# Optimization experiments

Hardware: AMD Instinct MI355X
Metric: run time of the kernel (lower is better)

Reference implementation:

```python
import jax, jax.numpy as jnp
import numpy as np

N, L, C_IN, NOISE_C, COMP, NC = 64, 1024, 514, 64, 16, 3
MAIN_C = COMP + NOISE_C  # 80

def _conv1d(x, w, b):
    # x: [N, Cin, L], w: [Cout, Cin, K] -> 'same' padding conv, stride 1
    k = w.shape[-1]
    y = jax.lax.conv_general_dilated(x, w, (1,), [(k // 2, k // 2)],
                                     dimension_numbers=('NCH', 'OIH', 'NCH'))
    return y + b[None, :, None]

def _bn(x, gamma, beta, eps=1e-5):
    # training-mode BatchNorm1d: biased batch stats over (N, L)
    mu = jnp.mean(x, axis=(0, 2), keepdims=True)
    var = jnp.var(x, axis=(0, 2), keepdims=True)
    return (x - mu) * jax.lax.rsqrt(var + eps) * gamma[None, :, None] + beta[None, :, None]

def _lrelu(x):
    return jax.nn.leaky_relu(x, 0.2)

def _pos_encode(length, dim, dtype):
    d = jnp.arange(dim)
    div = 1.0 / jnp.power(10000.0, (2.0 * (d // 2).astype(dtype)) / dim)  # [dim]
    ang = div[:, None] * jnp.arange(length, dtype=dtype)[None, :]          # [dim, L]
    pe = jnp.where((d % 2 == 0)[:, None], jnp.sin(ang), jnp.cos(ang))
    return pe[None].astype(dtype)  # [1, dim, L]

def _label_revise(probs):
    # Vectorized equivalent of the per-sample Python revision loop
    # (circle_itv=2, slider_itv=4, stride=2). Output length == input length.
    # Row j semantics (m = 4*(j//4), chain(m) = pred[m]==2 and pred[m+4]==2 and m+4<L):
    #   j%4==0: always probs[j]
    #   chain(m) and j%4!=0: pad [0,0,1]
    #   j%4==1 (not chain): pred[m] in {1,2} -> [1,0,0] else probs[j]
    #   j%4==2 (not chain): probs[j]
    #   j%4==3 (not chain): pred[j-1]==1 -> [1,0,0] else probs[j]
    n, l, c = probs.shape
    pred = jnp.argmax(probs, axis=-1)                 # [N, L]
    pred_b = pred[:, ::4]                              # pred at multiples of 4
    nxt = jnp.concatenate([pred_b[:, 1:], jnp.full((n, 1), -1, pred_b.dtype)], axis=1)
    chain = jnp.repeat((pred_b == 2) & (nxt == 2), 4, axis=1)   # [N, L]
    predm = jnp.repeat(pred_b, 4, axis=1)                        # [N, L]
    phase = jnp.arange(l) % 4
    prev = jnp.concatenate([jnp.zeros((n, 1), pred.dtype), pred[:, :-1]], axis=1)
    pad100 = jnp.array([1.0, 0.0, 0.0], probs.dtype)
    pad001 = jnp.array([0.0, 0.0, 1.0], probs.dtype)
    c100 = (((phase == 1)[None] & ((predm == 1) | (predm == 2)))
            | ((phase == 3)[None] & (prev == 1))) & ~chain
    out = jnp.where(c100[..., None], pad100, probs)
    out = jnp.where((chain & (phase != 0)[None])[..., None], pad001, out)
    return out

def _forward(noise, cond_data, gumbel, ew1, eb1, ew2, eb2, eg, ebt,
             w3, b3, w4, b4, g4, bt4, lw1, lb1, lw2, lb2, lw3, lb3):
    # FeatureExtractor
    x = jnp.swapaxes(cond_data, 1, 2)                       # [N, 514, L]
    x = _lrelu(_conv1d(x, ew1, eb1))                        # [N, 32, L]
    cond = _bn(_conv1d(x, ew2, eb2), eg, ebt)               # [N, 16, L] (no act)
    # main generator
    gi = jnp.concatenate([cond, jnp.swapaxes(noise, 1, 2)], axis=1)  # [N, 80, L]
    gi = gi + _pos_encode(L, MAIN_C, gi.dtype)
    h = _lrelu(_conv1d(gi, w3, b3))                         # [N, 48, L]
    h = _lrelu(_bn(_conv1d(h, w4, b4), g4, bt4))            # [N, 12, L]
    h = h.reshape(h.shape[0], -1)                           # [N, 12*L]
    h = _lrelu(h @ lw1 + lb1)
    h = _lrelu(h @ lw2 + lb2)
    logits = (h @ lw3 + lb3).reshape(-1, L, NC)             # [N, L, 3]
    rev = _label_revise(logits)
    # hard gumbel-softmax (tau=1) with straight-through estimator
    y_soft = jax.nn.softmax(rev + gumbel, axis=-1)
    y_hard = jax.nn.one_hot(jnp.argmax(y_soft, axis=-1), NC, dtype=y_soft.dtype)
    gen = y_hard + y_soft - jax.lax.stop_gradient(y_soft)
    return gen, cond

def setup_inputs() -> dict:
    key = jax.random.key(0)
    ks = jax.random.split(key, 12)
    s = jnp.float32(0.02)
    return {
        'noise': jax.random.normal(ks[0], (N, L, NOISE_C), jnp.float32),
        'cond_data': jax.random.normal(ks[1], (N, L, C_IN), jnp.float32),
        'gumbel': jax.random.gumbel(ks[2], (N, L, NC), jnp.float32),
        'ew1': jax.random.normal(ks[3], (C_IN // 16, C_IN, 1), jnp.float32) * s,
        'eb1': jnp.zeros((C_IN // 16,), jnp.float32),
        'ew2': jax.random.normal(ks[4], (COMP, C_IN // 16, 3), jnp.float32) * s,
        'eb2': jnp.zeros((COMP,), jnp.float32),
        'eg': jnp.ones((COMP,), jnp.float32),
        'ebt': jnp.zeros((COMP,), jnp.float32),
        'w3': jax.random.normal(ks[5], (NC * 16, MAIN_C, 7), jnp.float32) * s,
        'b3': jnp.zeros((NC * 16,), jnp.float32),
        'w4': jax.random.normal(ks[6], (NC * 4, NC * 16, 3), jnp.float32) * s,
        'b4': jnp.zeros((NC * 4,), jnp.float32),
        'g4': jnp.ones((NC * 4,), jnp.float32),
        'bt4': jnp.zeros((NC * 4,), jnp.float32),
        'lw1': jax.random.normal(ks[7], (NC * 4 * L, NC * L), jnp.float32) * s,
        'lb1': jnp.zeros((NC * L,), jnp.float32),
        'lw2': jax.random.normal(ks[8], (NC * L, NC * L), jnp.float32) * s,
        'lb2': jnp.zeros((NC * L,), jnp.float32),
        'lw3': jax.random.normal(ks[9], (NC * L, NC * L), jnp.float32) * s,
        'lb3': jnp.zeros((NC * L,), jnp.float32),
    }

def reference(noise, cond_data, gumbel, ew1, eb1, ew2, eb2, eg, ebt,
              w3, b3, w4, b4, g4, bt4, lw1, lb1, lw2, lb2, lw3, lb3):
    return _forward(noise, cond_data, gumbel, ew1, eb1, ew2, eb2, eg, ebt,
                    w3, b3, w4, b4, g4, bt4, lw1, lb1, lw2, lb2, lw3, lb3)
```

## Files before the change

kernel.cpp:

```cpp
#include <hip/hip_runtime.h>
#include <hip/hip_bf16.h>
#include <math.h>


__device__ __forceinline__ float lrelu(float x){ return fmaxf(x, 0.2f*x); }

__global__ void k_init(const float* __restrict__ ew1, const float* __restrict__ ew2,
                       const float* __restrict__ w3,  const float* __restrict__ w4,
                       float* __restrict__ wT1, float* __restrict__ wT2,
                       float* __restrict__ wT3, float* __restrict__ wT4,
                       float* __restrict__ pe){
  int i = blockIdx.x*256 + threadIdx.x;
  if (i < 16448){
    int c = i>>5, oc = i&31;
    wT1[i] = ew1[oc*514 + c];
  } else if (i < 16448+1536){
    int j = i - 16448; int oc = j%16; int t = j/16; int dl = t%3; int ic = t/3;
    wT2[j] = ew2[(oc*32+ic)*3 + dl];
  } else if (i < 16448+1536+26880){
    int j = i - 17984; int oc = j%48; int t = j/48; int dl = t%7; int ic = t/7;
    wT3[j] = w3[(oc*80+ic)*7 + dl];
  } else if (i < 46592){
    int j = i - 44864; int oc = j%12; int t = j/12; int dl = t%3; int ic = t/3;
    wT4[j] = w4[(oc*48+ic)*3 + dl];
  } else if (i < 46592 + 80*1024){
    int j = i - 46592;
    int ch = j >> 10, l = j & 1023;
    double dv = 1.0 / pow(10000.0, (2.0*(double)(ch>>1)) / 80.0);
    double ang = dv * (double)l;
    pe[j] = (float)((ch & 1) ? cos(ang) : sin(ang));
  }
}

__global__ __launch_bounds__(256) void k_conv1(const float* __restrict__ A,
    const float* __restrict__ wT1, const float* __restrict__ eb1,
    float* __restrict__ x1){
  __shared__ float red[32][256];
  const int tid = threadIdx.x;
  const int pl  = tid & 63;
  const int s   = __builtin_amdgcn_readfirstlane(tid >> 6);
  const int p   = blockIdx.x*64 + pl;

  const int c0 = (s == 0) ? 0 : 130 + (s-1)*128;
  const int c1 = (s == 0) ? 130 : 130 + s*128;

  const float* row = A + (size_t)p*514;
  float acc[32];
  #pragma unroll
  for (int j=0;j<32;j++) acc[j]=0.f;

  #pragma unroll 8
  for (int c=c0;c<c1;c+=2){
    float2 v = *reinterpret_cast<const float2*>(row + c);
    const float* w = wT1 + (size_t)c*32;
    #pragma unroll
    for (int j=0;j<32;j++) acc[j] = fmaf(v.x, w[j],    acc[j]);
    #pragma unroll
    for (int j=0;j<32;j++) acc[j] = fmaf(v.y, w[32+j], acc[j]);
  }

  #pragma unroll
  for (int j=0;j<32;j++) red[j][s*64 + pl] = acc[j];
  __syncthreads();

  float out[8];
  #pragma unroll
  for (int j=0;j<8;j++){
    const int c = s*8 + j;
    float v = (red[c][pl] + red[c][64+pl]) + (red[c][128+pl] + red[c][192+pl]);
    out[j] = lrelu(v + eb1[c]);
  }
  float* dst = x1 + ((size_t)(blockIdx.x*64 + pl))*32 + s*8;
  *(float4*)(dst  ) = make_float4(out[0],out[1],out[2],out[3]);
  *(float4*)(dst+4) = make_float4(out[4],out[5],out[6],out[7]);
}

__global__ __launch_bounds__(256) void k_conv2(const float* __restrict__ x1,
    const float* __restrict__ wT2, const float* __restrict__ eb2,
    float* __restrict__ y2, float* __restrict__ part){
  __shared__ float xt[32][264];
  const int tid = threadIdx.x, lane = tid & 63;
  const int wv = __builtin_amdgcn_readfirstlane(tid >> 6);
  const int n = blockIdx.x >> 2, base = (blockIdx.x & 3)*256;

  for (int r = tid; r < 264; r += 256){
    int l = base - 4 + r;
    if (l >= 0 && l < 1024){
      const float* src = x1 + ((size_t)n*1024 + l)*32;
      #pragma unroll
      for (int c=0;c<32;c+=4){
        float4 v = *(const float4*)(src + c);
        xt[c][r]=v.x; xt[c+1][r]=v.y; xt[c+2][r]=v.z; xt[c+3][r]=v.w;
      }
    } else {
      #pragma unroll
      for (int c=0;c<32;c++) xt[c][r] = 0.f;
    }
  }
  __syncthreads();

  const int og = wv*4;
  const int j0 = 4*lane;
  float acc[4][4];
  #pragma unroll
  for (int j=0;j<4;j++){
    #pragma unroll
    for (int p=0;p<4;p++) acc[j][p]=0.f;
  }
  for (int ic=0; ic<32; ic++){
    float xr[12];
    #pragma unroll
    for (int u=0;u<12;u+=4){
      float4 v = *(const float4*)&xt[ic][j0+u];
      xr[u]=v.x; xr[u+1]=v.y; xr[u+2]=v.z; xr[u+3]=v.w;
    }
    const float* wrow = wT2 + ic*48 + og;
    #pragma unroll
    for (int dl=0;dl<3;dl++){
      #pragma unroll
      for (int j=0;j<4;j++){
        float w = wrow[dl*16 + j];
        #pragma unroll
        for (int p=0;p<4;p++)
          acc[j][p] = fmaf(xr[p+dl+3], w, acc[j][p]);
      }
    }
  }
  float s[4], q[4];
  #pragma unroll
  for (int j=0;j<4;j++){ s[j]=0.f; q[j]=0.f; }
  const int l0 = base + 4*lane;
  #pragma unroll
  for (int p=0;p<4;p++){
    float vv[4];
    #pragma unroll
    for (int j=0;j<4;j++){
      float val = acc[j][p] + eb2[og+j];
      vv[j]=val; s[j]+=val; q[j]+=val*val;
    }
    *(float4*)(y2 + ((size_t)n*1024 + l0 + p)*16 + og) = make_float4(vv[0],vv[1],vv[2],vv[3]);
  }
  #pragma unroll
  for (int off=32; off; off>>=1){
    #pragma unroll
    for (int j=0;j<4;j++){ s[j] += __shfl_xor(s[j], off); q[j] += __shfl_xor(q[j], off); }
  }
  if (lane == 0){
    #pragma unroll
    for (int j=0;j<4;j++){
      part[((size_t)blockIdx.x*16 + og + j)*2    ] = s[j];
      part[((size_t)blockIdx.x*16 + og + j)*2 + 1] = q[j];
    }
  }
}

__global__ __launch_bounds__(256) void k_conv3(const float* __restrict__ y2,
    const float* __restrict__ noise, const float* __restrict__ pe,
    const float* __restrict__ bn2p, const float* __restrict__ eg,
    const float* __restrict__ ebt,
    const float* __restrict__ wT3, const float* __restrict__ b3,
    float* __restrict__ h3, float* __restrict__ cond_out){
  __shared__ float xt[80][72];
  __shared__ double pS[16][16], pQ[16][16];
  __shared__ float ssh[32];
  const int tid = threadIdx.x, lane = tid & 63;
  const int og = __builtin_amdgcn_readfirstlane(tid >> 6) * 12;
  const int n = blockIdx.x >> 4, base = (blockIdx.x & 15)*64;

  {
    int c = tid & 15, chunk = tid >> 4;
    double S=0.0, Q=0.0;
    #pragma unroll 4
    for (int i=chunk*16; i<chunk*16+16; i++){
      S += (double)bn2p[((size_t)i*16 + c)*2];
      Q += (double)bn2p[((size_t)i*16 + c)*2 + 1];
    }
    pS[chunk][c] = S; pQ[chunk][c] = Q;
  }
  __syncthreads();
  if (tid < 16){
    double S=0.0, Q=0.0;
    #pragma unroll
    for (int k=0;k<16;k++){ S += pS[k][tid]; Q += pQ[k][tid]; }
    double mean = S / 65536.0;
    double var  = Q / 65536.0 - mean*mean;
    double sc   = (double)eg[tid] / sqrt(var + 1e-5);
    ssh[tid*2]   = (float)sc;
    ssh[tid*2+1] = (float)((double)ebt[tid] - mean*sc);
  }
  __syncthreads();

  {
    const int q = tid & 3;
    for (int r = tid >> 2; r < 72; r += 64){
      int l = base - 4 + r;
      bool valid = (l >= 0 && l < 1024);
      if (q == 0){
        if (valid){
          size_t p = (size_t)n*1024 + l;
          const float* ys = y2 + p*16;
          bool interior = (r >= 4 && r < 68);
          #pragma unroll
          for (int c=0;c<16;c++){
            float cv = fmaf(ys[c], ssh[2*c], ssh[2*c+1]);
            if (interior) cond_out[((size_t)n*16 + c)*1024 + l] = cv;
            xt[c][r] = cv + pe[c*1024 + l];
          }
          const float* ns = noise + p*64;
          #pragma unroll
          for (int c=0;c<4;c++)
            xt[16+c][r] = ns[c] + pe[(16+c)*1024 + l];
        } else {
          #pragma unroll
          for (int c=0;c<20;c++) xt[c][r] = 0.f;
        }
      } else {
        if (valid){
          size_t p = (size_t)n*1024 + l;
          const float* ns = noise + p*64 + (q*20 - 16);
          #pragma unroll
          for (int c=0;c<20;c++)
            xt[q*20 + c][r] = ns[c] + pe[(q*20 + c)*1024 + l];
        } else {
          #pragma unroll
          for (int c=0;c<20;c++) xt[q*20 + c][r] = 0.f;
        }
      }
    }
  }
  __syncthreads();

  float acc[12];
  #pragma unroll
  for (int j=0;j<12;j++) acc[j]=0.f;
  for (int ic=0; ic<80; ic++){
    float xr[7];
    #pragma unroll
    for (int u=0;u<7;u++) xr[u] = xt[ic][lane+1+u];
    const float* wrow = wT3 + ic*336 + og;
    #pragma unroll
    for (int dl=0;dl<7;dl++){
      #pragma unroll
      for (int j=0;j<12;j++)
        acc[j] = fmaf(xr[dl], wrow[dl*48 + j], acc[j]);
    }
  }
  {
    float v[12];
    #pragma unroll
    for (int j=0;j<12;j++) v[j] = lrelu(acc[j] + b3[og+j]);
    float* dst = h3 + ((size_t)n*1024 + base + lane)*48 + og;
    *(float4*)(dst  ) = make_float4(v[0],v[1],v[2],v[3]);
    *(float4*)(dst+4) = make_float4(v[4],v[5],v[6],v[7]);
    *(float4*)(dst+8) = make_float4(v[8],v[9],v[10],v[11]);
  }
}

__global__ __launch_bounds__(256) void k_conv4(const float* __restrict__ h3,
    const float* __restrict__ wT4, const float* __restrict__ b4,
    float* __restrict__ y4, float* __restrict__ part){
  __shared__ float xt[48][258];
  __shared__ float red[4][24];
  const int tid = threadIdx.x, lane = tid & 63, wv = tid >> 6;
  const int n = blockIdx.x >> 2, base = (blockIdx.x & 3)*256;

  for (int r = tid; r < 258; r += 256){
    int l = base - 1 + r;
    if (l >= 0 && l < 1024){
      const float* src = h3 + ((size_t)n*1024 + l)*48;
      #pragma unroll
      for (int c=0;c<48;c+=4){
        float4 v = *(const float4*)(src + c);
        xt[c][r]=v.x; xt[c+1][r]=v.y; xt[c+2][r]=v.z; xt[c+3][r]=v.w;
      }
    } else {
      #pragma unroll
      for (int c=0;c<48;c++) xt[c][r]=0.f;
    }
  }
  __syncthreads();

  float acc[12];
  #pragma unroll
  for (int j=0;j<12;j++) acc[j]=0.f;
  for (int ic=0; ic<48; ic++){
    float x0 = xt[ic][tid], x1v = xt[ic][tid+1], x2 = xt[ic][tid+2];
    const float* wrow = wT4 + ic*36;
    #pragma unroll
    for (int j=0;j<12;j++){
      acc[j] = fmaf(x0,  wrow[j],      acc[j]);
      acc[j] = fmaf(x1v, wrow[12 + j], acc[j]);
      acc[j] = fmaf(x2,  wrow[24 + j], acc[j]);
    }
  }
  float s[12], q[12];
  #pragma unroll
  for (int j=0;j<12;j++){
    float v = acc[j] + b4[j];
    acc[j] = v; s[j] = v; q[j] = v*v;
  }
  {
    float* dst = y4 + ((size_t)n*1024 + base + tid)*12;
    *(float4*)(dst  ) = make_float4(acc[0],acc[1],acc[2],acc[3]);
    *(float4*)(dst+4) = make_float4(acc[4],acc[5],acc[6],acc[7]);
    *(float4*)(dst+8) = make_float4(acc[8],acc[9],acc[10],acc[11]);
  }
  #pragma unroll
  for (int off=32; off; off>>=1){
    #pragma unroll
    for (int j=0;j<12;j++){ s[j] += __shfl_xor(s[j], off); q[j] += __shfl_xor(q[j], off); }
  }
  if (lane == 0){
    #pragma unroll
    for (int j=0;j<12;j++){ red[wv][j] = s[j]; red[wv][12+j] = q[j]; }
  }
  __syncthreads();
  if (tid < 24){
    float v = red[0][tid] + red[1][tid] + red[2][tid] + red[3][tid];
    if (tid < 12) part[((size_t)blockIdx.x*12 + tid)*2] = v;
    else          part[((size_t)blockIdx.x*12 + (tid-12))*2 + 1] = v;
  }
}

__global__ __launch_bounds__(256) void k_hflat(const float* __restrict__ y4,
    const float* __restrict__ bn4p, const float* __restrict__ g4,
    const float* __restrict__ bt4, float* __restrict__ hT){
  __shared__ double pS[16][12], pQ[16][12];
  __shared__ float ssh[24];
  const int tid = threadIdx.x;
  if (tid < 192){
    int c = tid % 12, chunk = tid / 12;
    double S=0.0, Q=0.0;
    #pragma unroll 4
    for (int i=chunk*16; i<chunk*16+16; i++){
      S += (double)bn4p[((size_t)i*12 + c)*2];
      Q += (double)bn4p[((size_t)i*12 + c)*2 + 1];
    }
    pS[chunk][c] = S; pQ[chunk][c] = Q;
  }
  __syncthreads();
  if (tid < 12){
    double S=0.0, Q=0.0;
    #pragma unroll
    for (int k=0;k<16;k++){ S += pS[k][tid]; Q += pQ[k][tid]; }
    double mean = S / 65536.0;
    double var  = Q / 65536.0 - mean*mean;
    double sc   = (double)g4[tid] / sqrt(var + 1e-5);
    ssh[tid*2]   = (float)sc;
    ssh[tid*2+1] = (float)((double)bt4[tid] - mean*sc);
  }
  __syncthreads();

  int nn = tid & 63;
  int l  = blockIdx.x*4 + (tid >> 6);
  const float* src = y4 + ((size_t)nn*1024 + l)*12;
  #pragma unroll
  for (int c=0;c<12;c++){
    float v = lrelu(fmaf(src[c], ssh[2*c], ssh[2*c+1]));
    hT[((size_t)(c*1024 + l))*64 + nn] = v;
  }
}

__global__ __launch_bounds__(256) void k_fc2(const float* __restrict__ AT,
    const float* __restrict__ W, float* __restrict__ part,
    int nsplit, int kwave){
  __shared__ float red[64][64];
  const int lane = threadIdx.x & 63;
  const int w  = __builtin_amdgcn_readfirstlane(threadIdx.x >> 6);
  const int sk = w >> 1;
  const int mh = (w & 1) * 32;
  const int s  = blockIdx.x % nsplit;
  const int ot = blockIdx.x / nsplit;
  const int o  = ot*64 + lane;
  const int k0 = (s*2 + sk) * kwave;

  float acc[32];
  #pragma unroll
  for (int m=0;m<32;m++) acc[m]=0.f;

  const float* ap = AT + (size_t)k0*64 + mh;
  const float* wp = W  + (size_t)k0*3072 + o;

  float wb[8];
  #pragma unroll
  for (int u=0;u<8;u++) wb[u] = wp[(size_t)u*3072];

  for (int k=0; k<kwave-8; k+=8){
    float wn[8];
    const float* wpn = wp + (size_t)(k+8)*3072;
    #pragma unroll
    for (int u=0;u<8;u++) wn[u] = wpn[(size_t)u*3072];
    #pragma unroll
    for (int u=0;u<8;u++){
      const float* a = ap + (size_t)(k+u)*64;
      #pragma unroll
      for (int m=0;m<32;m++) acc[m] = fmaf(a[m], wb[u], acc[m]);
    }
    #pragma unroll
    for (int u=0;u<8;u++) wb[u] = wn[u];
  }
  #pragma unroll
  for (int u=0;u<8;u++){
    const float* a = ap + (size_t)(kwave-8+u)*64;
    #pragma unroll
    for (int m=0;m<32;m++) acc[m] = fmaf(a[m], wb[u], acc[m]);
  }

  if (sk == 1){
    #pragma unroll
    for (int m=0;m<32;m++) red[mh + m][lane] = acc[m];
  }
  __syncthreads();
  if (sk == 0){
    float* dst = part + (size_t)s*64*3072 + o;
    #pragma unroll
    for (int m=0;m<32;m++){
      acc[m] += red[mh + m][lane];
      dst[(size_t)(mh + m)*3072] = acc[m];
    }
  }
}

__global__ __launch_bounds__(256) void k_fcreduce(const float* __restrict__ part,
    const float* __restrict__ bias, float* __restrict__ out,
    int S, int act, int transposed){
  const int ot = blockIdx.x >> 4;
  const int mg = blockIdx.x & 15;
  const int lane = threadIdx.x & 63;
  const int o = ot*64 + lane;
  const int m = mg*4 + (threadIdx.x >> 6);
  float v = 0.f;
  for (int s=0;s<S;s++) v += part[((size_t)s*64 + m)*3072 + o];
  v += bias[o];
  if (act) v = fmaxf(v, 0.2f*v);
  if (transposed) out[(size_t)o*64 + m] = v;
  else            out[(size_t)m*3072 + o] = v;
}

__global__ __launch_bounds__(256) void k_label(const float* __restrict__ logits,
    const float* __restrict__ gumbel, float* __restrict__ out){
  __shared__ int pred[1024];
  const int n = blockIdx.x;
  const float* lg = logits + (size_t)n*3072;
  for (int l = threadIdx.x; l < 1024; l += 256){
    float a = lg[l*3], b = lg[l*3+1], c = lg[l*3+2];
    int pm = 0; float bv = a;
    if (b > bv){ pm = 1; bv = b; }
    if (c > bv){ pm = 2; }
    pred[l] = pm;
  }
  __syncthreads();
  const float* gm = gumbel + (size_t)n*3072;
  float* op = out + (size_t)n*3072;
  for (int l = threadIdx.x; l < 1024; l += 256){
    int phase = l & 3, lb = l >> 2;
    int pb  = pred[lb*4];
    int nxt = (lb < 255) ? pred[(lb+1)*4] : -1;
    bool chain = (pb == 2) && (nxt == 2);
    int prev = (l > 0) ? pred[l-1] : 0;
    bool c100 = (((phase == 1) && (pb == 1 || pb == 2)) ||
                 ((phase == 3) && (prev == 1))) && !chain;
    float r0, r1, r2;
    if (chain && phase != 0){ r0=0.f; r1=0.f; r2=1.f; }
    else if (c100)          { r0=1.f; r1=0.f; r2=0.f; }
    else { r0 = lg[l*3]; r1 = lg[l*3+1]; r2 = lg[l*3+2]; }
    float z0 = r0 + gm[l*3], z1 = r1 + gm[l*3+1], z2 = r2 + gm[l*3+2];
    int am = 0; float bv = z0;
    if (z1 > bv){ am = 1; bv = z1; }
    if (z2 > bv){ am = 2; }
    op[l*3+0] = (am == 0) ? 1.f : 0.f;
    op[l*3+1] = (am == 1) ? 1.f : 0.f;
    op[l*3+2] = (am == 2) ? 1.f : 0.f;
  }
}

extern "C" void kernel_launch(void* const* d_in, const int* in_sizes, int n_in,
                              void* d_out, int out_size, void* d_ws, size_t ws_size,
                              hipStream_t stream){
  (void)in_sizes; (void)n_in; (void)out_size;
  const float* noise     = (const float*)d_in[0];
  const float* cond_data = (const float*)d_in[1];
  const float* gumbel    = (const float*)d_in[2];
  const float* ew1 = (const float*)d_in[3];
  const float* eb1 = (const float*)d_in[4];
  const float* ew2 = (const float*)d_in[5];
  const float* eb2 = (const float*)d_in[6];
  const float* eg  = (const float*)d_in[7];
  const float* ebt = (const float*)d_in[8];
  const float* w3  = (const float*)d_in[9];
  const float* b3  = (const float*)d_in[10];
  const float* w4  = (const float*)d_in[11];
  const float* b4  = (const float*)d_in[12];
  const float* g4  = (const float*)d_in[13];
  const float* bt4 = (const float*)d_in[14];
  const float* lw1 = (const float*)d_in[15];
  const float* lb1 = (const float*)d_in[16];
  const float* lw2 = (const float*)d_in[17];
  const float* lb2 = (const float*)d_in[18];
  const float* lw3 = (const float*)d_in[19];
  const float* lb3 = (const float*)d_in[20];

  float* ws = (float*)d_ws;
  float* wT1   = ws + 0;
  float* wT2   = ws + 16448;
  float* wT3   = ws + 17984;
  float* wT4   = ws + 44864;
  float* pe    = ws + 46592;
  float* bn2p  = ws + 128512;
  float* bn4p  = ws + 136736;
  float* x1    = ws + 143360;
  float* y2    = ws + 2240512;
  float* h3    = ws + 3289088;
  float* y4    = ws + 6434816;
  float* hT    = ws + 7221248;
  float* fcp   = ws + 8007680;

  int S1 = 32;
  if (ws_size < (size_t)(8007680 + 32*196608 + 3*196608) * 4) S1 = 16;
  const int S23 = 16;
  float* fc1T  = fcp + (size_t)S1*196608;
  float* fc2T  = fc1T + 196608;
  float* logi  = fc2T + 196608;
  const int kw1  = 12288 / (S1*2);
  const int kw23 = 3072 / (S23*2);

  float* out_gen  = (float*)d_out;
  float* out_cond = (float*)d_out + 196608;

  k_init <<<502, 256, 0, stream>>>(ew1, ew2, w3, w4, wT1, wT2, wT3, wT4, pe);
  k_conv1<<<1024, 256, 0, stream>>>(cond_data, wT1, eb1, x1);
  k_conv2<<<256, 256, 0, stream>>>(x1, wT2, eb2, y2, bn2p);
  k_conv3<<<1024, 256, 0, stream>>>(y2, noise, pe, bn2p, eg, ebt, wT3, b3, h3, out_cond);
  k_conv4<<<256, 256, 0, stream>>>(h3, wT4, b4, y4, bn4p);
  k_hflat<<<256, 256, 0, stream>>>(y4, bn4p, g4, bt4, hT);
  k_fc2  <<<48*S1, 256, 0, stream>>>(hT,   lw1, fcp, S1, kw1);
  k_fcreduce<<<768, 256, 0, stream>>>(fcp, lb1, fc1T, S1, 1, 1);
  k_fc2  <<<48*S23, 256, 0, stream>>>(fc1T, lw2, fcp, S23, kw23);
  k_fcreduce<<<768, 256, 0, stream>>>(fcp, lb2, fc2T, S23, 1, 1);
  k_fc2  <<<48*S23, 256, 0, stream>>>(fc2T, lw3, fcp, S23, kw23);
  k_fcreduce<<<768, 256, 0, stream>>>(fcp, lb3, logi, S23, 0, 0);
  k_label<<<64, 256, 0, stream>>>(logi, gumbel, out_gen);
}
```

Measured before the change: 325.2 us.

## Stage FC activation tiles in LDS and deepen FC1 split-K

Adds a new FC kernel that copies the activation slice for its K range into shared memory once per block, then streams weight rows with register double-buffering over a fixed K chunk of 96. FC1 now uses 64 K-splits instead of 32, and FC2/FC3 use the new kernel. The aim is to raise parallelism and cut repeated global reads of activations for these memory-bound GEMVs. In exchange it adds LDS pressure and more partial sums for the reduce kernel to read. It keeps the old kernel as a fallback when the workspace is too small.

```diff
diff --git a/kernel.cpp b/kernel.cpp
--- a/kernel.cpp
+++ b/kernel.cpp
@@ -421,6 +421,78 @@
   }
 }
 
+__global__ __launch_bounds__(256) void k_fc6(const float* __restrict__ AT,
+    const float* __restrict__ W, float* __restrict__ part,
+    int nsplit){
+  const int kwave = 96;
+  __shared__ float als[2*96*64];
+  const int tid  = threadIdx.x;
+  const int lane = tid & 63;
+  const int w  = __builtin_amdgcn_readfirstlane(tid >> 6);
+  const int sk = w >> 1;
+  const int mh = (w & 1) * 32;
+  const int s  = blockIdx.x % nsplit;
+  const int ot = blockIdx.x / nsplit;
+  const int o  = ot*64 + lane;
+  const int k0 = (s*2 + sk) * kwave;
+
+  {
+    const float4* src = (const float4*)(AT + (size_t)(s*2*kwave)*64);
+    float4* dst = (float4*)als;
+    #pragma unroll
+    for (int i=0;i<12;i++)
+      dst[tid + i*256] = src[tid + i*256];
+  }
+  __syncthreads();
+
+  float acc[32];
+  #pragma unroll
+  for (int m=0;m<32;m++) acc[m]=0.f;
+
+  const float* ap = als + (sk*kwave)*64 + mh;
+  const float* wp = W + (size_t)k0*3072 + o;
+
+  float wb[8];
+  #pragma unroll
+  for (int u=0;u<8;u++) wb[u] = wp[(size_t)u*3072];
+
+  for (int k=0; k<kwave-8; k+=8){
+    float wn[8];
+    const float* wpn = wp + (size_t)(k+8)*3072;
+    #pragma unroll
+    for (int u=0;u<8;u++) wn[u] = wpn[(size_t)u*3072];
+    #pragma unroll
+    for (int u=0;u<8;u++){
+      const float* a = ap + (k+u)*64;
+      #pragma unroll
+      for (int m=0;m<32;m++) acc[m] = fmaf(a[m], wb[u], acc[m]);
+    }
+    #pragma unroll
+    for (int u=0;u<8;u++) wb[u] = wn[u];
+  }
+  #pragma unroll
+  for (int u=0;u<8;u++){
+    const float* a = ap + (kwave-8+u)*64;
+    #pragma unroll
+    for (int m=0;m<32;m++) acc[m] = fmaf(a[m], wb[u], acc[m]);
+  }
+
+  __syncthreads();
+  if (sk == 1){
+    #pragma unroll
+    for (int m=0;m<32;m++) als[(mh+m)*64 + lane] = acc[m];
+  }
+  __syncthreads();
+  if (sk == 0){
+    float* dst = part + (size_t)s*64*3072 + o;
+    #pragma unroll
+    for (int m=0;m<32;m++){
+      acc[m] += als[(mh+m)*64 + lane];
+      dst[(size_t)(mh+m)*3072] = acc[m];
+    }
+  }
+}
+
 __global__ __launch_bounds__(256) void k_fcreduce(const float* __restrict__ part,
     const float* __restrict__ bias, float* __restrict__ out,
     int S, int act, int transposed){
@@ -515,14 +587,15 @@
   float* hT    = ws + 7221248;
   float* fcp   = ws + 8007680;
 
-  int S1 = 32;
-  if (ws_size < (size_t)(8007680 + 32*196608 + 3*196608) * 4) S1 = 16;
+  int S1 = 64;
+  bool lds_fc1 = true;
+  if (ws_size < (size_t)(8007680 + (size_t)64*196608 + 3*196608) * 4){
+    S1 = 32; lds_fc1 = false;
+  }
   const int S23 = 16;
   float* fc1T  = fcp + (size_t)S1*196608;
   float* fc2T  = fc1T + 196608;
   float* logi  = fc2T + 196608;
-  const int kw1  = 12288 / (S1*2);
-  const int kw23 = 3072 / (S23*2);
 
   float* out_gen  = (float*)d_out;
   float* out_cond = (float*)d_out + 196608;
@@ -533,11 +606,12 @@
   k_conv3<<<1024, 256, 0, stream>>>(y2, noise, pe, bn2p, eg, ebt, wT3, b3, h3, out_cond);
   k_conv4<<<256, 256, 0, stream>>>(h3, wT4, b4, y4, bn4p);
   k_hflat<<<256, 256, 0, stream>>>(y4, bn4p, g4, bt4, hT);
-  k_fc2  <<<48*S1, 256, 0, stream>>>(hT,   lw1, fcp, S1, kw1);
+  if (lds_fc1) k_fc6<<<48*64, 256, 0, stream>>>(hT, lw1, fcp, 64);
+  else         k_fc2<<<48*32, 256, 0, stream>>>(hT, lw1, fcp, 32, 192);
   k_fcreduce<<<768, 256, 0, stream>>>(fcp, lb1, fc1T, S1, 1, 1);
-  k_fc2  <<<48*S23, 256, 0, stream>>>(fc1T, lw2, fcp, S23, kw23);
+  k_fc6  <<<48*16, 256, 0, stream>>>(fc1T, lw2, fcp, 16);
   k_fcreduce<<<768, 256, 0, stream>>>(fcp, lb2, fc2T, S23, 1, 1);
-  k_fc2  <<<48*S23, 256, 0, stream>>>(fc2T, lw3, fcp, S23, kw23);
+  k_fc6  <<<48*16, 256, 0, stream>>>(fc2T, lw3, fcp, 16);
   k_fcreduce<<<768, 256, 0, stream>>>(fcp, lb3, logi, S23, 0, 0);
   k_label<<<64, 256, 0, stream>>>(logi, gumbel, out_gen);
 }
```

Measured after the change: 380.2 us. +16.9%, slower.

## Stage FC activation tiles in LDS and raise split-K for FC2/FC3

Applied to the files above, without the earlier changes.

The FC GEMV-like kernel now copies 48-row chunks of the transposed activation matrix into shared memory with float4 loads, in phases. Each wave then reads the chunk from LDS rather than re-reading global/L1 per lane. Split-K for the second and third FC layers goes from 16 to 32 to put more blocks on the device. The workspace size fallback is removed, so the code now assumes the workspace is large enough for 32 partials. More syncs and more partial-reduce traffic are added in exchange.

```diff
diff --git a/kernel.cpp b/kernel.cpp
--- a/kernel.cpp
+++ b/kernel.cpp
@@ -361,12 +361,14 @@
   }
 }
 
-__global__ __launch_bounds__(256) void k_fc2(const float* __restrict__ AT,
-    const float* __restrict__ W, float* __restrict__ part,
-    int nsplit, int kwave){
-  __shared__ float red[64][64];
-  const int lane = threadIdx.x & 63;
-  const int w  = __builtin_amdgcn_readfirstlane(threadIdx.x >> 6);
+template<int NPH>
+__global__ __launch_bounds__(256) void k_fc7(const float* __restrict__ AT,
+    const float* __restrict__ W, float* __restrict__ part, int nsplit){
+  const int kwave = NPH*48;
+  __shared__ float als[2*48*64];
+  const int tid  = threadIdx.x;
+  const int lane = tid & 63;
+  const int w  = __builtin_amdgcn_readfirstlane(tid >> 6);
   const int sk = w >> 1;
   const int mh = (w & 1) * 32;
   const int s  = blockIdx.x % nsplit;
@@ -378,45 +380,61 @@
   #pragma unroll
   for (int m=0;m<32;m++) acc[m]=0.f;
 
-  const float* ap = AT + (size_t)k0*64 + mh;
-  const float* wp = W  + (size_t)k0*3072 + o;
-
+  const float* wp = W + (size_t)k0*3072 + o;
   float wb[8];
   #pragma unroll
   for (int u=0;u<8;u++) wb[u] = wp[(size_t)u*3072];
 
-  for (int k=0; k<kwave-8; k+=8){
-    float wn[8];
-    const float* wpn = wp + (size_t)(k+8)*3072;
-    #pragma unroll
-    for (int u=0;u<8;u++) wn[u] = wpn[(size_t)u*3072];
-    #pragma unroll
-    for (int u=0;u<8;u++){
-      const float* a = ap + (size_t)(k+u)*64;
-      #pragma unroll
-      for (int m=0;m<32;m++) acc[m] = fmaf(a[m], wb[u], acc[m]);
-    }
-    #pragma unroll
-    for (int u=0;u<8;u++) wb[u] = wn[u];
-  }
-  #pragma unroll
-  for (int u=0;u<8;u++){
-    const float* a = ap + (size_t)(kwave-8+u)*64;
-    #pragma unroll
-    for (int m=0;m<32;m++) acc[m] = fmaf(a[m], wb[u], acc[m]);
-  }
-
+  for (int ph=0; ph<NPH; ++ph){
+    __syncthreads();
+    {
+      const float4* s0 = (const float4*)(AT + ((size_t)(s*2    )*kwave + ph*48)*64);
+      const float4* s1 = (const float4*)(AT + ((size_t)(s*2 + 1)*kwave + ph*48)*64);
+      float4* d = (float4*)als;
+      #pragma unroll
+      for (int i=0;i<3;i++){
+        d[tid + i*256]       = s0[tid + i*256];
+        d[768 + tid + i*256] = s1[tid + i*256];
+      }
+    }
+    __syncthreads();
+
+    const float* ap = als + sk*48*64 + mh;
+    #pragma unroll
+    for (int g=0; g<6; ++g){
+      const int kk = ph*48 + g*8;
+      float wn[8];
+      const bool pref = (kk + 8 < kwave);
+      if (pref){
+        const float* wpn = wp + (size_t)(kk+8)*3072;
+        #pragma unroll
+        for (int u=0;u<8;u++) wn[u] = wpn[(size_t)u*3072];
+      }
+      #pragma unroll
+      for (int u=0;u<8;u++){
+        const float* a = ap + (g*8+u)*64;
+        #pragma unroll
+        for (int m=0;m<32;m++) acc[m] = fmaf(a[m], wb[u], acc[m]);
+      }
+      if (pref){
+        #pragma unroll
+        for (int u=0;u<8;u++) wb[u] = wn[u];
+      }
+    }
+  }
+
+  __syncthreads();
   if (sk == 1){
     #pragma unroll
-    for (int m=0;m<32;m++) red[mh + m][lane] = acc[m];
+    for (int m=0;m<32;m++) als[(mh+m)*64 + lane] = acc[m];
   }
   __syncthreads();
   if (sk == 0){
     float* dst = part + (size_t)s*64*3072 + o;
     #pragma unroll
     for (int m=0;m<32;m++){
-      acc[m] += red[mh + m][lane];
-      dst[(size_t)(mh + m)*3072] = acc[m];
+      acc[m] += als[(mh+m)*64 + lane];
+      dst[(size_t)(mh+m)*3072] = acc[m];
     }
   }
 }
@@ -477,7 +495,7 @@
 extern "C" void kernel_launch(void* const* d_in, const int* in_sizes, int n_in,
                               void* d_out, int out_size, void* d_ws, size_t ws_size,
                               hipStream_t stream){
-  (void)in_sizes; (void)n_in; (void)out_size;
+  (void)in_sizes; (void)n_in; (void)out_size; (void)ws_size;
   const float* noise     = (const float*)d_in[0];
   const float* cond_data = (const float*)d_in[1];
   const float* gumbel    = (const float*)d_in[2];
@@ -515,14 +533,11 @@
   float* hT    = ws + 7221248;
   float* fcp   = ws + 8007680;
 
-  int S1 = 32;
-  if (ws_size < (size_t)(8007680 + 32*196608 + 3*196608) * 4) S1 = 16;
-  const int S23 = 16;
-  float* fc1T  = fcp + (size_t)S1*196608;
+  const int S1  = 32;
+  const int S23 = 32;
+  float* fc1T  = fcp + (size_t)32*196608;
   float* fc2T  = fc1T + 196608;
   float* logi  = fc2T + 196608;
-  const int kw1  = 12288 / (S1*2);
-  const int kw23 = 3072 / (S23*2);
 
   float* out_gen  = (float*)d_out;
   float* out_cond = (float*)d_out + 196608;
@@ -533,11 +548,11 @@
   k_conv3<<<1024, 256, 0, stream>>>(y2, noise, pe, bn2p, eg, ebt, wT3, b3, h3, out_cond);
   k_conv4<<<256, 256, 0, stream>>>(h3, wT4, b4, y4, bn4p);
   k_hflat<<<256, 256, 0, stream>>>(y4, bn4p, g4, bt4, hT);
-  k_fc2  <<<48*S1, 256, 0, stream>>>(hT,   lw1, fcp, S1, kw1);
+  k_fc7<4><<<48*S1, 256, 0, stream>>>(hT,   lw1, fcp, S1);
   k_fcreduce<<<768, 256, 0, stream>>>(fcp, lb1, fc1T, S1, 1, 1);
-  k_fc2  <<<48*S23, 256, 0, stream>>>(fc1T, lw2, fcp, S23, kw23);
+  k_fc7<1><<<48*S23, 256, 0, stream>>>(fc1T, lw2, fcp, S23);
   k_fcreduce<<<768, 256, 0, stream>>>(fcp, lb2, fc2T, S23, 1, 1);
-  k_fc2  <<<48*S23, 256, 0, stream>>>(fc2T, lw3, fcp, S23, kw23);
+  k_fc7<1><<<48*S23, 256, 0, stream>>>(fc2T, lw3, fcp, S23);
   k_fcreduce<<<768, 256, 0, stream>>>(fcp, lb3, logi, S23, 0, 0);
   k_label<<<64, 256, 0, stream>>>(logi, gumbel, out_gen);
 }
```

Result: slower. 349.7 us (+7.5%).
